# Kernel optimization log

Measured on AMD Instinct MI355X. Metric: run time of the kernel, lower is better.

## Reference

```python
import jax, jax.numpy as jnp
import numpy as np

N = 100000   # nodes
E = 1600000  # edges
IN = 128
HID = 128
OUT = 40
EPS = 1e-5


def setup_inputs() -> dict:
    key = jax.random.key(0)
    ks = jax.random.split(key, 8)
    x = jax.random.normal(ks[0], (N, IN), jnp.float32)
    edge_index = jax.random.randint(ks[1], (2, E), 0, N, dtype=jnp.int32)
    W1 = jax.random.normal(ks[2], (IN, HID), jnp.float32) / np.float32(np.sqrt(IN))
    b1 = jnp.zeros((HID,), jnp.float32)
    g1 = jnp.ones((HID,), jnp.float32)
    be1 = jnp.zeros((HID,), jnp.float32)
    W2 = jax.random.normal(ks[3], (HID, HID), jnp.float32) / np.float32(np.sqrt(HID))
    b2 = jnp.zeros((HID,), jnp.float32)
    g2 = jnp.ones((HID,), jnp.float32)
    be2 = jnp.zeros((HID,), jnp.float32)
    W3 = jax.random.normal(ks[4], (HID, OUT), jnp.float32) / np.float32(np.sqrt(HID))
    b3 = jnp.zeros((OUT,), jnp.float32)
    return dict(x=x, edge_index=edge_index, W1=W1, b1=b1, g1=g1, be1=be1,
                W2=W2, b2=b2, g2=g2, be2=be2, W3=W3, b3=b3)


def _gcn_norm(edge_index, n):
    # PyG gcn_norm: add self loops, symmetric D^-1/2 (A+I) D^-1/2 weights
    loop = jnp.arange(n, dtype=edge_index.dtype)
    src = jnp.concatenate([edge_index[0], loop])
    dst = jnp.concatenate([edge_index[1], loop])
    deg = jax.ops.segment_sum(jnp.ones_like(dst, jnp.float32), dst, num_segments=n)
    dinv = jnp.where(deg > 0, jax.lax.rsqrt(deg), 0.0)
    norm = dinv[src] * dinv[dst]  # [E+N]
    return src, dst, norm


def _gcn_conv(x, W, b, src, dst, norm, n):
    h = x @ W                                   # [N, F]
    msg = h[src] * norm[:, None]                # gather + scale  [E+N, F]
    agg = jax.ops.segment_sum(msg, dst, num_segments=n)
    return agg + b


def _batchnorm(x, g, be):
    mu = jnp.mean(x, axis=0)
    var = jnp.var(x, axis=0)
    return (x - mu) * jax.lax.rsqrt(var + EPS) * g + be


def reference(x, edge_index, W1, b1, g1, be1, W2, b2, g2, be2, W3, b3):
    n = x.shape[0]
    src, dst, norm = _gcn_norm(edge_index, n)
    h = _gcn_conv(x, W1, b1, src, dst, norm, n)
    h = jax.nn.relu(_batchnorm(h, g1, be1))
    h = _gcn_conv(h, W2, b2, src, dst, norm, n)
    h = jax.nn.relu(_batchnorm(h, g2, be2))
    h = _gcn_conv(h, W3, b3, src, dst, norm, n)
    return jax.nn.softmax(h, axis=-1)
```

## Files before the change

kernel.cpp:

```cpp
#include <hip/hip_runtime.h>
#include <hip/hip_fp16.h>

#define NN   100000
#define NE   1600000
#define NBUCK 391
#define NW1   512
#define CH1   (NE / NW1)
#define GN    (NBUCK * NW1)
#define SC    512
#define SNB   (GN / SC)
#define BNB   512
constexpr float EPSV = 1e-5f;

typedef _Float16 f16x8 __attribute__((ext_vector_type(8)));
typedef float    f32x4 __attribute__((ext_vector_type(4)));


__global__ __launch_bounds__(256) void p1hist_kernel(const int* __restrict__ dst,
                                                     int* __restrict__ G) {
    __shared__ int h[NBUCK];
    int t = threadIdx.x, wg = blockIdx.x;
    for (int i = t; i < NBUCK; i += 256) h[i] = 0;
    __syncthreads();
    int base = wg * CH1;
    for (int e = base + t; e < base + CH1; e += 256)
        atomicAdd(&h[dst[e] >> 8], 1);
    __syncthreads();
    for (int i = t; i < NBUCK; i += 256) G[i * NW1 + wg] = h[i];
}

__global__ __launch_bounds__(256) void gscan1_kernel(const int* __restrict__ G,
                                                     int* __restrict__ bsum) {
    __shared__ int red[256];
    int t = threadIdx.x;
    int base = blockIdx.x * SC + t * 2;
    red[t] = G[base] + G[base + 1];
    __syncthreads();
    #pragma unroll
    for (int off = 128; off > 0; off >>= 1) {
        if (t < off) red[t] += red[t + off];
        __syncthreads();
    }
    if (t == 0) bsum[blockIdx.x] = red[0];
}

__global__ __launch_bounds__(256) void gscan3_kernel(int* __restrict__ G,
                                                     const int* __restrict__ bsum) {
    __shared__ int pre[256];
    __shared__ int s[256];
    int t = threadIdx.x;
    int part = 0;
    for (int j = t; j < (int)blockIdx.x; j += 256) part += bsum[j];
    pre[t] = part;
    __syncthreads();
    #pragma unroll
    for (int off = 128; off > 0; off >>= 1) {
        if (t < off) pre[t] += pre[t + off];
        __syncthreads();
    }
    int boffv = pre[0];
    int base = blockIdx.x * SC + t * 2;
    int c0 = G[base], c1 = G[base + 1];
    int pair = c0 + c1;
    s[t] = pair;
    __syncthreads();
    #pragma unroll
    for (int off = 1; off < 256; off <<= 1) {
        int u = (t >= off) ? s[t - off] : 0;
        __syncthreads();
        s[t] += u;
        __syncthreads();
    }
    int excl = boffv + s[t] - pair;
    G[base]     = excl;
    G[base + 1] = excl + c0;
}

__global__ __launch_bounds__(256) void p1fill_kernel(const int* __restrict__ src,
                                                     const int* __restrict__ dst,
                                                     const int* __restrict__ G,
                                                     int* __restrict__ ebuf) {
    __shared__ int cur[NBUCK];
    int t = threadIdx.x, wg = blockIdx.x;
    for (int i = t; i < NBUCK; i += 256) cur[i] = G[i * NW1 + wg];
    __syncthreads();
    int base = wg * CH1;
    for (int e = base + t; e < base + CH1; e += 256) {
        int d = dst[e];
        int pos = atomicAdd(&cur[d >> 8], 1);
        ebuf[pos] = src[e] | ((d & 255) << 17);
    }
}

__global__ __launch_bounds__(256) void p2build_kernel(const int* __restrict__ ebuf,
                                                      const int* __restrict__ G,
                                                      int* __restrict__ rowptr,
                                                      int* __restrict__ srcsorted,
                                                      float* __restrict__ dinv) {
    __shared__ int cnt[256];
    __shared__ int s[256];
    __shared__ int cur[256];
    int t = threadIdx.x, b = blockIdx.x;
    int base = G[b * NW1];
    int endp = (b == NBUCK - 1) ? NE : G[(b + 1) * NW1];
    cnt[t] = 0;
    __syncthreads();
    for (int e = base + t; e < endp; e += 256)
        atomicAdd(&cnt[ebuf[e] >> 17], 1);
    __syncthreads();
    int c = cnt[t];
    s[t] = c;
    __syncthreads();
    #pragma unroll
    for (int off = 1; off < 256; off <<= 1) {
        int u = (t >= off) ? s[t - off] : 0;
        __syncthreads();
        s[t] += u;
        __syncthreads();
    }
    int excl = s[t] - c;
    int node = b * 256 + t;
    if (node < NN) {
        rowptr[node] = base + excl;
        dinv[node]   = rsqrtf((float)c + 1.0f);
    }
    cur[t] = base + excl;
    __syncthreads();
    for (int e = base + t; e < endp; e += 256) {
        int p = ebuf[e];
        int pos = atomicAdd(&cur[p >> 17], 1);
        srcsorted[pos] = p & 0x1FFFF;
    }
    if (b == NBUCK - 1 && t == 0) rowptr[NN] = NE;
}


__global__ void wprep_kernel(const float* __restrict__ W1, const float* __restrict__ W2,
                             __half* __restrict__ Wt) {
    int b = blockIdx.x;
    int layer = b >> 7, n = b & 127, k = threadIdx.x;
    const float* W = layer ? W2 : W1;
    Wt[layer * 16384 + n * 128 + k] = __float2half_rn(W[k * 128 + n]);
}


__global__ __launch_bounds__(256) void bnstats_kernel(const __half* __restrict__ X,
                                                      float* __restrict__ partial) {
    __shared__ float red[4][256];
    int t = threadIdx.x;
    int f2 = t & 63, rg = t >> 6;
    const __half2* base = (const __half2*)X + f2;
    float s0 = 0.f, s1 = 0.f, q0 = 0.f, q1 = 0.f;
    for (int r = blockIdx.x * 4 + rg; r < NN; r += BNB * 4) {
        float2 v = __half22float2(base[(size_t)r * 64]);
        s0 += v.x; s1 += v.y; q0 += v.x * v.x; q1 += v.y * v.y;
    }
    red[rg][f2 * 4 + 0] = s0;
    red[rg][f2 * 4 + 1] = s1;
    red[rg][f2 * 4 + 2] = q0;
    red[rg][f2 * 4 + 3] = q1;
    __syncthreads();
    int kind = t >> 7, f = t & 127;
    int slot = (f >> 1) * 4 + (f & 1) + kind * 2;
    float v = red[0][slot] + red[1][slot] + red[2][slot] + red[3][slot];
    partial[blockIdx.x * 256 + kind * 128 + f] = v;
}

__global__ __launch_bounds__(256) void bnfinal_kernel(const float* __restrict__ partial,
                                                      const float* __restrict__ g,
                                                      const float* __restrict__ be,
                                                      float* __restrict__ sc) {
    __shared__ float red[256];
    int t = threadIdx.x;
    float v = 0.f;
    #pragma unroll 8
    for (int sl = 0; sl < BNB; ++sl) v += partial[sl * 256 + t];
    red[t] = v;
    __syncthreads();
    if (t < 128) {
        float s = red[t], q = red[128 + t];
        float mu  = s * (1.0f / NN);
        float var = q * (1.0f / NN) - mu * mu;
        float rstd = rsqrtf(var + EPSV);
        float scale = g[t] * rstd;
        sc[t]       = scale;
        sc[128 + t] = be[t] - mu * scale;
    }
}


__device__ __forceinline__ int swzb(int row, int colByte) {
    return row * 256 + (colByte ^ ((row & 7) << 4));
}

template<bool BN, typename TIN>
__global__ __launch_bounds__(256) void gemm128m_kernel(const TIN* __restrict__ X,
        const __half* __restrict__ Wt, const float* __restrict__ sc,
        const float* __restrict__ dinv, __half* __restrict__ Y) {
    __shared__ __align__(16) char Xs[64 * 256];
    __shared__ __align__(16) char Wts[128 * 256];
    __shared__ float dvs[64];
    int tid = threadIdx.x;
    int node0 = blockIdx.x * 64;

    {
        int n = tid >> 1, c0 = (tid & 1) * 64;
        const _Float16* g = (const _Float16*)Wt + n * 128 + c0;
        #pragma unroll
        for (int j = 0; j < 8; ++j) {
            f16x8 v = *(const f16x8*)(g + j * 8);
            *(f16x8*)(Wts + swzb(n, (c0 + j * 8) * 2)) = v;
        }
    }
    {
        int r = tid >> 2, c0 = (tid & 3) * 32;
        int grow = node0 + r;
        #pragma unroll
        for (int j = 0; j < 4; ++j) {
            int c = c0 + j * 8;
            f16x8 o;
            if (grow < NN) {
                float f[8];
                if constexpr (sizeof(TIN) == 4) {
                    float4 u0 = *(const float4*)((const float*)X + (size_t)grow * 128 + c);
                    float4 u1 = *(const float4*)((const float*)X + (size_t)grow * 128 + c + 4);
                    f[0] = u0.x; f[1] = u0.y; f[2] = u0.z; f[3] = u0.w;
                    f[4] = u1.x; f[5] = u1.y; f[6] = u1.z; f[7] = u1.w;
                } else {
                    f16x8 h = *(const f16x8*)((const _Float16*)X + (size_t)grow * 128 + c);
                    #pragma unroll
                    for (int i = 0; i < 8; ++i) f[i] = (float)h[i];
                }
                #pragma unroll
                for (int i = 0; i < 8; ++i) {
                    if constexpr (BN) f[i] = fmaxf(fmaf(f[i], sc[c + i], sc[128 + c + i]), 0.f);
                    o[i] = (_Float16)f[i];
                }
            } else {
                #pragma unroll
                for (int i = 0; i < 8; ++i) o[i] = (_Float16)0.f;
            }
            *(f16x8*)(Xs + swzb(r, c * 2)) = o;
        }
    }
    if (tid < 64) dvs[tid] = (node0 + tid < NN) ? dinv[node0 + tid] : 0.f;
    __syncthreads();

    int lane = tid & 63;
    int wv   = tid >> 6;
    int n0w  = wv * 32;
    int lm   = lane & 15;
    int lg   = lane >> 4;

    f32x4 acc[4][2] = {};
    #pragma unroll
    for (int s = 0; s < 4; ++s) {
        int kb = (s * 32 + lg * 8) * 2;
        f16x8 a[4], b[2];
        #pragma unroll
        for (int i = 0; i < 4; ++i)
            a[i] = *(const f16x8*)(Xs + swzb(i * 16 + lm, kb));
        #pragma unroll
        for (int r = 0; r < 2; ++r)
            b[r] = *(const f16x8*)(Wts + swzb(n0w + r * 16 + lm, kb));
        #pragma unroll
        for (int i = 0; i < 4; ++i)
            #pragma unroll
            for (int r = 0; r < 2; ++r)
                acc[i][r] = __builtin_amdgcn_mfma_f32_16x16x32_f16(a[i], b[r], acc[i][r], 0, 0, 0);
    }

    _Float16* Yh = (_Float16*)Y;
    #pragma unroll
    for (int i = 0; i < 4; ++i) {
        #pragma unroll
        for (int q = 0; q < 4; ++q) {
            int row = i * 16 + lg * 4 + q;
            int grow = node0 + row;
            if (grow < NN) {
                float di = dvs[row];
                Yh[(size_t)grow * 128 + n0w + lm]      = (_Float16)(acc[i][0][q] * di);
                Yh[(size_t)grow * 128 + n0w + 16 + lm] = (_Float16)(acc[i][1][q] * di);
            }
        }
    }
}


__global__ __launch_bounds__(256) void gemm40_kernel(const __half* __restrict__ X,
        const float* __restrict__ W, const float* __restrict__ sc,
        const float* __restrict__ dinv, __half* __restrict__ Y) {
    __shared__ float Ws[128][40];
    __shared__ float Xs[32][132];
    int tx = threadIdx.x, ty = threadIdx.y;
    int tid = ty * 8 + tx;
    int node0 = blockIdx.x * 32;

    float* wf = &Ws[0][0];
    for (int idx = tid; idx < 128 * 40; idx += 256) wf[idx] = W[idx];
    for (int idx = tid * 8; idx < 32 * 128; idx += 256 * 8) {
        int n = idx >> 7, f = idx & 127;
        f16x8 h = *(const f16x8*)((const _Float16*)X + (size_t)(node0 + n) * 128 + f);
        float v[8];
        #pragma unroll
        for (int i = 0; i < 8; ++i)
            v[i] = fmaxf(fmaf((float)h[i], sc[f + i], sc[128 + f + i]), 0.f);
        *(float4*)&Xs[n][f]     = make_float4(v[0], v[1], v[2], v[3]);
        *(float4*)&Xs[n][f + 4] = make_float4(v[4], v[5], v[6], v[7]);
    }
    __syncthreads();

    float acc[5] = {0, 0, 0, 0, 0};
    int f0 = tx * 5;
    #pragma unroll 4
    for (int k = 0; k < 128; ++k) {
        float xv = Xs[ty][k];
        #pragma unroll
        for (int j = 0; j < 5; ++j) acc[j] = fmaf(xv, Ws[k][f0 + j], acc[j]);
    }
    float di = dinv[node0 + ty];
    __half* yp = Y + (size_t)(node0 + ty) * 40;
    #pragma unroll
    for (int j = 0; j < 5; ++j) yp[f0 + j] = __float2half_rn(acc[j] * di);
}


__global__ __launch_bounds__(256) void agg128_kernel(const __half* __restrict__ H,
        const int* __restrict__ rowptr, const int* __restrict__ srcs,
        const float* __restrict__ dinv, const float* __restrict__ bias,
        __half* __restrict__ Bout) {
    int wave = threadIdx.x >> 6;
    int lane = threadIdx.x & 63;
    int node = blockIdx.x * 4 + wave;
    int beg = rowptr[node], end = rowptr[node + 1];
    int g = lane >> 4;
    int c = lane & 15;
    const f16x8* Hc = (const f16x8*)H + c;
    float acc[8] = {};
    int e = beg;
    for (; e + 7 < end; e += 8) {
        int s0 = srcs[e + g];
        int s1 = srcs[e + 4 + g];
        f16x8 h0 = Hc[(size_t)s0 * 16];
        f16x8 h1 = Hc[(size_t)s1 * 16];
        #pragma unroll
        for (int j = 0; j < 8; ++j) {
            acc[j] = fmaf((float)h0[j], 1.0f, acc[j]);
            acc[j] = fmaf((float)h1[j], 1.0f, acc[j]);
        }
    }
    for (; e + 3 < end; e += 4) {
        int s0 = srcs[e + g];
        f16x8 h0 = Hc[(size_t)s0 * 16];
        #pragma unroll
        for (int j = 0; j < 8; ++j) acc[j] = fmaf((float)h0[j], 1.0f, acc[j]);
    }
    if (e + g < end) {
        int s = srcs[e + g];
        f16x8 h = Hc[(size_t)s * 16];
        #pragma unroll
        for (int j = 0; j < 8; ++j) acc[j] = fmaf((float)h[j], 1.0f, acc[j]);
    }
    #pragma unroll
    for (int j = 0; j < 8; ++j) {
        acc[j] += __shfl_xor(acc[j], 16);
        acc[j] += __shfl_xor(acc[j], 32);
    }
    float di = dinv[node];
    f16x8 hs = Hc[(size_t)node * 16];
    _Float16 o[8];
    #pragma unroll
    for (int j = 0; j < 8; ++j) {
        float v = di * (acc[j] + (float)hs[j]) + bias[c * 8 + j];
        o[j] = (_Float16)v;
    }
    if (g == 0)
        *((f16x8*)Bout + (size_t)node * 16 + c) = *(f16x8*)o;
}


__global__ __launch_bounds__(256) void agg40_softmax_kernel(const __half* __restrict__ H,
        const int* __restrict__ rowptr, const int* __restrict__ srcs,
        const float* __restrict__ dinv, const float* __restrict__ bias,
        float* __restrict__ out) {
    int wave = threadIdx.x >> 6;
    int lane = threadIdx.x & 63;
    int node = blockIdx.x * 4 + wave;
    int beg = rowptr[node], end = rowptr[node + 1];
    bool act = lane < 40;
    int ln = act ? lane : 0;
    const _Float16* Hc = (const _Float16*)H + ln;
    float a0 = 0.f, a1 = 0.f, a2 = 0.f, a3 = 0.f;
    float a4 = 0.f, a5 = 0.f, a6 = 0.f, a7 = 0.f;
    int e = beg;
    for (; e + 7 < end; e += 8) {
        a0 = fmaf((float)Hc[(size_t)srcs[e]     * 40], 1.0f, a0);
        a1 = fmaf((float)Hc[(size_t)srcs[e + 1] * 40], 1.0f, a1);
        a2 = fmaf((float)Hc[(size_t)srcs[e + 2] * 40], 1.0f, a2);
        a3 = fmaf((float)Hc[(size_t)srcs[e + 3] * 40], 1.0f, a3);
        a4 = fmaf((float)Hc[(size_t)srcs[e + 4] * 40], 1.0f, a4);
        a5 = fmaf((float)Hc[(size_t)srcs[e + 5] * 40], 1.0f, a5);
        a6 = fmaf((float)Hc[(size_t)srcs[e + 6] * 40], 1.0f, a6);
        a7 = fmaf((float)Hc[(size_t)srcs[e + 7] * 40], 1.0f, a7);
    }
    if (e + 3 < end) {
        a0 = fmaf((float)Hc[(size_t)srcs[e]     * 40], 1.0f, a0);
        a1 = fmaf((float)Hc[(size_t)srcs[e + 1] * 40], 1.0f, a1);
        a2 = fmaf((float)Hc[(size_t)srcs[e + 2] * 40], 1.0f, a2);
        a3 = fmaf((float)Hc[(size_t)srcs[e + 3] * 40], 1.0f, a3);
        e += 4;
    }
    for (; e < end; ++e) a0 = fmaf((float)Hc[(size_t)srcs[e] * 40], 1.0f, a0);
    float di = dinv[node];
    float hs = (float)Hc[(size_t)node * 40];
    float v = act ? (di * (a0 + a1 + a2 + a3 + a4 + a5 + a6 + a7 + hs) + bias[lane]) : -3.0e38f;
    float m = v;
    #pragma unroll
    for (int off = 32; off > 0; off >>= 1) m = fmaxf(m, __shfl_xor(m, off));
    float ev = act ? expf(v - m) : 0.f;
    float ssum = ev;
    #pragma unroll
    for (int off = 32; off > 0; off >>= 1) ssum += __shfl_xor(ssum, off);
    if (act) out[(size_t)node * 40 + lane] = ev / ssum;
}


extern "C" void kernel_launch(void* const* d_in, const int* in_sizes, int n_in,
                              void* d_out, int out_size, void* d_ws, size_t ws_size,
                              hipStream_t stream) {
    const float* x   = (const float*)d_in[0];
    const int*   ei  = (const int*)d_in[1];
    const float* W1  = (const float*)d_in[2];
    const float* b1  = (const float*)d_in[3];
    const float* g1  = (const float*)d_in[4];
    const float* be1 = (const float*)d_in[5];
    const float* W2  = (const float*)d_in[6];
    const float* b2  = (const float*)d_in[7];
    const float* g2  = (const float*)d_in[8];
    const float* be2 = (const float*)d_in[9];
    const float* W3  = (const float*)d_in[10];
    const float* b3  = (const float*)d_in[11];
    float* out = (float*)d_out;
    const int* src = ei;
    const int* dst = ei + NE;

    char* p = (char*)d_ws;
    auto alloc = [&](size_t bytes) { char* r = p; p += (bytes + 255) & ~255ull; return r; };
    int*    rowptr    = (int*)   alloc((size_t)(NN + 1) * 4);
    int*    srcsorted = (int*)   alloc((size_t)NE * 4);
    float*  dinv      = (float*) alloc((size_t)NN * 4);
    float*  sc        = (float*) alloc(256 * 4);
    int*    G         = (int*)   alloc((size_t)GN * 4);
    int*    bsum      = (int*)   alloc((size_t)SNB * 4);
    float*  partial   = (float*) alloc((size_t)BNB * 256 * 4);
    __half* Wth       = (__half*)alloc((size_t)2 * 16384 * 2);
    __half* A         = (__half*)alloc((size_t)NN * 128 * 2);
    __half* Bh        = (__half*)alloc((size_t)NN * 128 * 2);
    int*    ebuf      = (int*)A;

    wprep_kernel<<<256, 128, 0, stream>>>(W1, W2, Wth);
    p1hist_kernel<<<NW1, 256, 0, stream>>>(dst, G);
    gscan1_kernel<<<SNB, 256, 0, stream>>>(G, bsum);
    gscan3_kernel<<<SNB, 256, 0, stream>>>(G, bsum);
    p1fill_kernel<<<NW1, 256, 0, stream>>>(src, dst, G, ebuf);
    p2build_kernel<<<NBUCK, 256, 0, stream>>>(ebuf, G, rowptr, srcsorted, dinv);

    const int GB = (NN + 63) / 64;
    gemm128m_kernel<false, float><<<GB, 256, 0, stream>>>(x, Wth, nullptr, dinv, A);
    agg128_kernel<<<NN / 4, 256, 0, stream>>>(A, rowptr, srcsorted, dinv, b1, Bh);
    bnstats_kernel<<<BNB, 256, 0, stream>>>(Bh, partial);
    bnfinal_kernel<<<1, 256, 0, stream>>>(partial, g1, be1, sc);
    gemm128m_kernel<true, __half><<<GB, 256, 0, stream>>>(Bh, Wth + 16384, sc, dinv, A);
    agg128_kernel<<<NN / 4, 256, 0, stream>>>(A, rowptr, srcsorted, dinv, b2, Bh);
    bnstats_kernel<<<BNB, 256, 0, stream>>>(Bh, partial);
    bnfinal_kernel<<<1, 256, 0, stream>>>(partial, g2, be2, sc);
    gemm40_kernel<<<NN / 32, dim3(8, 32), 0, stream>>>(Bh, W3, sc, dinv, A);
    agg40_softmax_kernel<<<NN / 4, 256, 0, stream>>>(A, rowptr, srcsorted, dinv, b3, out);
}
```

Before: 401.3 us.

## Read GEMM weights from global directly, widen agg unroll, use plain adds

```diff
diff --git a/kernel.cpp b/kernel.cpp
--- a/kernel.cpp
+++ b/kernel.cpp
@@ -198,20 +198,10 @@
         const __half* __restrict__ Wt, const float* __restrict__ sc,
         const float* __restrict__ dinv, __half* __restrict__ Y) {
     __shared__ __align__(16) char Xs[64 * 256];
-    __shared__ __align__(16) char Wts[128 * 256];
     __shared__ float dvs[64];
     int tid = threadIdx.x;
     int node0 = blockIdx.x * 64;
 
-    {
-        int n = tid >> 1, c0 = (tid & 1) * 64;
-        const _Float16* g = (const _Float16*)Wt + n * 128 + c0;
-        #pragma unroll
-        for (int j = 0; j < 8; ++j) {
-            f16x8 v = *(const f16x8*)(g + j * 8);
-            *(f16x8*)(Wts + swzb(n, (c0 + j * 8) * 2)) = v;
-        }
-    }
     {
         int r = tid >> 2, c0 = (tid & 3) * 32;
         int grow = node0 + r;
@@ -251,18 +241,19 @@
     int n0w  = wv * 32;
     int lm   = lane & 15;
     int lg   = lane >> 4;
+    const _Float16* Wg = (const _Float16*)Wt;
 
     f32x4 acc[4][2] = {};
     #pragma unroll
     for (int s = 0; s < 4; ++s) {
-        int kb = (s * 32 + lg * 8) * 2;
+        int kk = s * 32 + lg * 8;
         f16x8 a[4], b[2];
         #pragma unroll
+        for (int r = 0; r < 2; ++r)
+            b[r] = *(const f16x8*)(Wg + (size_t)(n0w + r * 16 + lm) * 128 + kk);
+        #pragma unroll
         for (int i = 0; i < 4; ++i)
-            a[i] = *(const f16x8*)(Xs + swzb(i * 16 + lm, kb));
-        #pragma unroll
-        for (int r = 0; r < 2; ++r)
-            b[r] = *(const f16x8*)(Wts + swzb(n0w + r * 16 + lm, kb));
+            a[i] = *(const f16x8*)(Xs + swzb(i * 16 + lm, kk * 2));
         #pragma unroll
         for (int i = 0; i < 4; ++i)
             #pragma unroll
@@ -338,28 +329,38 @@
     const f16x8* Hc = (const f16x8*)H + c;
     float acc[8] = {};
     int e = beg;
+    for (; e + 15 < end; e += 16) {
+        int s0 = srcs[e + g];
+        int s1 = srcs[e + 4 + g];
+        int s2 = srcs[e + 8 + g];
+        int s3 = srcs[e + 12 + g];
+        f16x8 h0 = Hc[(size_t)s0 * 16];
+        f16x8 h1 = Hc[(size_t)s1 * 16];
+        f16x8 h2 = Hc[(size_t)s2 * 16];
+        f16x8 h3 = Hc[(size_t)s3 * 16];
+        #pragma unroll
+        for (int j = 0; j < 8; ++j)
+            acc[j] += ((float)h0[j] + (float)h1[j]) + ((float)h2[j] + (float)h3[j]);
+    }
     for (; e + 7 < end; e += 8) {
         int s0 = srcs[e + g];
         int s1 = srcs[e + 4 + g];
         f16x8 h0 = Hc[(size_t)s0 * 16];
         f16x8 h1 = Hc[(size_t)s1 * 16];
         #pragma unroll
-        for (int j = 0; j < 8; ++j) {
-            acc[j] = fmaf((float)h0[j], 1.0f, acc[j]);
-            acc[j] = fmaf((float)h1[j], 1.0f, acc[j]);
-        }
+        for (int j = 0; j < 8; ++j) acc[j] += (float)h0[j] + (float)h1[j];
     }
     for (; e + 3 < end; e += 4) {
         int s0 = srcs[e + g];
         f16x8 h0 = Hc[(size_t)s0 * 16];
         #pragma unroll
-        for (int j = 0; j < 8; ++j) acc[j] = fmaf((float)h0[j], 1.0f, acc[j]);
+        for (int j = 0; j < 8; ++j) acc[j] += (float)h0[j];
     }
     if (e + g < end) {
         int s = srcs[e + g];
         f16x8 h = Hc[(size_t)s * 16];
         #pragma unroll
-        for (int j = 0; j < 8; ++j) acc[j] = fmaf((float)h[j], 1.0f, acc[j]);
+        for (int j = 0; j < 8; ++j) acc[j] += (float)h[j];
     }
     #pragma unroll
     for (int j = 0; j < 8; ++j) {
@@ -394,23 +395,23 @@
     float a4 = 0.f, a5 = 0.f, a6 = 0.f, a7 = 0.f;
     int e = beg;
     for (; e + 7 < end; e += 8) {
-        a0 = fmaf((float)Hc[(size_t)srcs[e]     * 40], 1.0f, a0);
-        a1 = fmaf((float)Hc[(size_t)srcs[e + 1] * 40], 1.0f, a1);
-        a2 = fmaf((float)Hc[(size_t)srcs[e + 2] * 40], 1.0f, a2);
-        a3 = fmaf((float)Hc[(size_t)srcs[e + 3] * 40], 1.0f, a3);
-        a4 = fmaf((float)Hc[(size_t)srcs[e + 4] * 40], 1.0f, a4);
-        a5 = fmaf((float)Hc[(size_t)srcs[e + 5] * 40], 1.0f, a5);
-        a6 = fmaf((float)Hc[(size_t)srcs[e + 6] * 40], 1.0f, a6);
-        a7 = fmaf((float)Hc[(size_t)srcs[e + 7] * 40], 1.0f, a7);
+        a0 += (float)Hc[(size_t)srcs[e]     * 40];
+        a1 += (float)Hc[(size_t)srcs[e + 1] * 40];
+        a2 += (float)Hc[(size_t)srcs[e + 2] * 40];
+        a3 += (float)Hc[(size_t)srcs[e + 3] * 40];
+        a4 += (float)Hc[(size_t)srcs[e + 4] * 40];
+        a5 += (float)Hc[(size_t)srcs[e + 5] * 40];
+        a6 += (float)Hc[(size_t)srcs[e + 6] * 40];
+        a7 += (float)Hc[(size_t)srcs[e + 7] * 40];
     }
     if (e + 3 < end) {
-        a0 = fmaf((float)Hc[(size_t)srcs[e]     * 40], 1.0f, a0);
-        a1 = fmaf((float)Hc[(size_t)srcs[e + 1] * 40], 1.0f, a1);
-        a2 = fmaf((float)Hc[(size_t)srcs[e + 2] * 40], 1.0f, a2);
-        a3 = fmaf((float)Hc[(size_t)srcs[e + 3] * 40], 1.0f, a3);
+        a0 += (float)Hc[(size_t)srcs[e]     * 40];
+        a1 += (float)Hc[(size_t)srcs[e + 1] * 40];
+        a2 += (float)Hc[(size_t)srcs[e + 2] * 40];
+        a3 += (float)Hc[(size_t)srcs[e + 3] * 40];
         e += 4;
     }
-    for (; e < end; ++e) a0 = fmaf((float)Hc[(size_t)srcs[e] * 40], 1.0f, a0);
+    for (; e < end; ++e) a0 += (float)Hc[(size_t)srcs[e] * 40];
     float di = dinv[node];
     float hs = (float)Hc[(size_t)node * 40];
     float v = act ? (di * (a0 + a1 + a2 + a3 + a4 + a5 + a6 + a7 + hs) + bias[lane]) : -3.0e38f;
```

Result: no change. 398.2 us (-0.8%).
